# Performance work log

Measured on AMD Instinct MI355X. Metric: run time of the kernel, lower is better.

Reference implementation:

```python
import jax, jax.numpy as jnp
import numpy as np

HID, STEM, BN_OUT, STEM_OUT, MLP = 256, 64, 128, 64, 128
BN_WS, STEM_WS = 5, 17
N, H_BN, W_BN, H_VIS, W_VIS = 4096, 128, 128, 1024, 1024


def setup_inputs() -> dict:
    key = jax.random.key(0)
    ks = jax.random.split(key, 24)
    f32 = jnp.float32
    def rn(k, shape, s=0.05):
        return jax.random.normal(k, shape, f32) * s
    return dict(
        bottleneck=rn(ks[0], (1, HID, H_BN, W_BN), 1.0),
        vis_stem_features=rn(ks[1], (1, STEM, H_VIS, W_VIS), 1.0),
        source_positions_vis=jax.random.uniform(ks[2], (N, 2), f32, 10.0, W_VIS - 10.0),
        pixel_to_sky=rn(ks[3], (N, 2, 2), 0.1),
        fused_h=H_BN, fused_w=W_BN, vis_h=H_VIS, vis_w=W_VIS,
        dw_w=rn(ks[4], (HID, 1, 7, 7)), dw_b=rn(ks[5], (HID,)),
        ln_g=jnp.ones((HID,), f32), ln_b=jnp.zeros((HID,), f32),
        pw1_w=rn(ks[6], (4 * HID, HID)), pw1_b=rn(ks[7], (4 * HID,)),
        pw2_w=rn(ks[8], (HID, 4 * HID)), pw2_b=rn(ks[9], (HID,)),
        cn_gamma=jnp.full((HID,), 1e-2, f32),
        bn1x1_w=rn(ks[10], (BN_OUT, HID, 1, 1)), bn1x1_b=rn(ks[11], (BN_OUT,)),
        st1_w=rn(ks[12], (STEM_OUT, STEM, 3, 3)), st1_b=rn(ks[13], (STEM_OUT,)),
        st2_w=rn(ks[14], (STEM_OUT, STEM_OUT, 3, 3)), st2_b=rn(ks[15], (STEM_OUT,)),
        h1_w=rn(ks[16], (MLP, BN_OUT + STEM_OUT)), h1_b=rn(ks[17], (MLP,)),
        h2_w=rn(ks[18], (MLP, MLP)), h2_b=rn(ks[19], (MLP,)),
        h3_w=rn(ks[20], (3, MLP)),
        h3_b=jnp.array([0.0, 0.0, float(np.log(0.05))], f32),
    )


def _gelu(x):
    return jax.nn.gelu(x, approximate=False)


def _conv2d(x, w, b, padding, groups=1):
    y = jax.lax.conv_general_dilated(
        x, w, (1, 1), [(padding, padding), (padding, padding)],
        dimension_numbers=('NCHW', 'OIHW', 'NCHW'), feature_group_count=groups)
    return y + b[None, :, None, None]


def _bilinear_windows(fm, pos, ws):
    """fm [1,C,H,W], pos [N,2] pixel coords -> [N,C,ws,ws].
    Matches torch grid_sample(mode=bilinear, padding=zeros, align_corners=True)
    with the module's normalize/unnormalize, i.e. direct pixel-coord sampling."""
    C, H, W = fm.shape[1:]
    fm2 = fm[0]
    half = ws // 2
    off = jnp.arange(-half, half + 1, dtype=pos.dtype)
    gy, gx = jnp.meshgrid(off, off, indexing='ij')
    xs = gx[None] + pos[:, 0, None, None]   # [N,ws,ws]
    ys = gy[None] + pos[:, 1, None, None]
    x0 = jnp.floor(xs); y0 = jnp.floor(ys)
    wx1 = xs - x0; wy1 = ys - y0
    x0i = x0.astype(jnp.int32); y0i = y0.astype(jnp.int32)
    def gather(yi, xi, w):
        valid = (yi >= 0) & (yi < H) & (xi >= 0) & (xi < W)
        v = fm2[:, jnp.clip(yi, 0, H - 1), jnp.clip(xi, 0, W - 1)]  # [C,N,ws,ws]
        return v * (w * valid)[None]
    out = (gather(y0i, x0i, (1 - wy1) * (1 - wx1))
           + gather(y0i, x0i + 1, (1 - wy1) * wx1)
           + gather(y0i + 1, x0i, wy1 * (1 - wx1))
           + gather(y0i + 1, x0i + 1, wy1 * wx1))
    return jnp.transpose(out, (1, 0, 2, 3))


def _gauss(ws):
    t = jnp.linspace(-1.0, 1.0, ws)
    yy, xx = jnp.meshgrid(t, t, indexing='ij')
    g = jnp.exp(-(xx ** 2 + yy ** 2) / (2 * 0.4 ** 2))
    return g / g.sum()


def _convnext(x, dw_w, dw_b, ln_g, ln_b, pw1_w, pw1_b, pw2_w, pw2_b, gamma):
    r = x
    x = _conv2d(x, dw_w, dw_b, padding=3, groups=x.shape[1])  # depthwise 7x7
    mu = x.mean(1, keepdims=True)
    var = ((x - mu) ** 2).mean(1, keepdims=True)
    x = (x - mu) / jnp.sqrt(var + 1e-6)
    x = x * ln_g[None, :, None, None] + ln_b[None, :, None, None]
    x = jnp.einsum('nchw,oc->nohw', x, pw1_w) + pw1_b[None, :, None, None]
    x = _gelu(x)
    x = jnp.einsum('nchw,oc->nohw', x, pw2_w) + pw2_b[None, :, None, None]
    return r + gamma[None, :, None, None] * x


def _forward(bottleneck, vis_stem_features, source_positions_vis, pixel_to_sky,
             dw_w, dw_b, ln_g, ln_b, pw1_w, pw1_b, pw2_w, pw2_b, cn_gamma,
             bn1x1_w, bn1x1_b, st1_w, st1_b, st2_w, st2_b,
             h1_w, h1_b, h2_w, h2_b, h3_w, h3_b,
             fused_h, fused_w, vis_h, vis_w):
    scale = jnp.array([fused_w / vis_w, fused_h / vis_h], source_positions_vis.dtype)
    pos_bn = source_positions_vis * scale
    # bottleneck branch: 5x5 windows -> ConvNeXt -> 1x1 conv -> GELU -> gauss pool
    bn_win = _bilinear_windows(bottleneck, pos_bn, BN_WS)              # [N,256,5,5]
    bn_feat = _convnext(bn_win, dw_w, dw_b, ln_g, ln_b, pw1_w, pw1_b, pw2_w, pw2_b, cn_gamma)
    bn_feat = _gelu(_conv2d(bn_feat, bn1x1_w, bn1x1_b, padding=0))     # [N,128,5,5]
    bn_vec = (bn_feat * _gauss(BN_WS)[None, None]).sum((-2, -1))       # [N,128]
    st_win = _bilinear_windows(vis_stem_features, source_positions_vis, STEM_WS)
    st = _gelu(_conv2d(st_win, st1_w, st1_b, padding=1))
    st = _gelu(_conv2d(st, st2_w, st2_b, padding=1))                   # [N,64,17,17]
    st_vec = (st * _gauss(STEM_WS)[None, None]).sum((-2, -1))          # [N,64]
    # head MLP
    x = jnp.concatenate([bn_vec, st_vec], axis=1)                      # [N,192]
    x = _gelu(x @ h1_w.T + h1_b)
    x = _gelu(x @ h2_w.T + h2_b)
    out = x @ h3_w.T + h3_b                                            # [N,3]
    dx_px, dy_px = out[:, 0], out[:, 1]
    log_sigma = jnp.clip(out[:, 2], -6.0, 3.0)
    pix = jnp.stack([dx_px, dy_px], axis=1)                            # [N,2]
    pred_sky = jnp.einsum('nij,nj->ni', pixel_to_sky, pix)             # [N,2]
    confidence = 1.0 / jnp.maximum(jnp.exp(log_sigma), 1e-4)
    return pred_sky, dx_px, dy_px, log_sigma, confidence


def reference(bottleneck, vis_stem_features, source_positions_vis, pixel_to_sky,
              fused_h, fused_w, vis_h, vis_w,
              dw_w, dw_b, ln_g, ln_b, pw1_w, pw1_b, pw2_w, pw2_b, cn_gamma,
              bn1x1_w, bn1x1_b, st1_w, st1_b, st2_w, st2_b,
              h1_w, h1_b, h2_w, h2_b, h3_w, h3_b):
    return _forward(bottleneck, vis_stem_features, source_positions_vis, pixel_to_sky,
                    dw_w, dw_b, ln_g, ln_b, pw1_w, pw1_b, pw2_w, pw2_b, cn_gamma,
                    bn1x1_w, bn1x1_b, st1_w, st1_b, st2_w, st2_b,
                    h1_w, h1_b, h2_w, h2_b, h3_w, h3_b,
                    fused_h, fused_w, vis_h, vis_w)
```

## Files before the change

### kernel.cpp

```cpp
#include <hip/hip_runtime.h>
#include <hip/hip_bf16.h>

#define XSTR 28

typedef short short8 __attribute__((ext_vector_type(8)));
typedef float f32x4  __attribute__((ext_vector_type(4)));

__device__ __forceinline__ float gelu_f(float x){
    return 0.5f*x*(1.0f + erff(x*0.70710678118654752f));
}
__device__ __forceinline__ float gelu_q(float x){
    const float z = 1.5957691216057308f*x*(1.0f + 0.044715f*x*x);
    return x / (1.0f + __expf(-z));
}
__device__ __forceinline__ unsigned short f2bf(float f){
    unsigned int u = __float_as_uint(f);
    u += 0x7fffu + ((u>>16)&1u);
    return (unsigned short)(u>>16);
}
__device__ __forceinline__ unsigned int pack2(float a, float b){
    return (unsigned int)f2bf(a) | ((unsigned int)f2bf(b)<<16);
}
__device__ __forceinline__ float bf_lo(unsigned int u){ return __uint_as_float(u<<16); }
__device__ __forceinline__ float bf_hi(unsigned int u){ return __uint_as_float(u & 0xffff0000u); }
__device__ __forceinline__ float bfu(unsigned short v){ return __uint_as_float(((unsigned int)v)<<16); }

__device__ __forceinline__ void fma_row25(const float* __restrict__ row, float w, float* __restrict__ acc){
    const float4* r4 = (const float4*)row;
    float4 a0=r4[0], a1=r4[1], a2=r4[2], a3=r4[3], a4=r4[4], a5=r4[5];
    float a6 = row[24];
    acc[0]+=a0.x*w;  acc[1]+=a0.y*w;  acc[2]+=a0.z*w;  acc[3]+=a0.w*w;
    acc[4]+=a1.x*w;  acc[5]+=a1.y*w;  acc[6]+=a1.z*w;  acc[7]+=a1.w*w;
    acc[8]+=a2.x*w;  acc[9]+=a2.y*w;  acc[10]+=a2.z*w; acc[11]+=a2.w*w;
    acc[12]+=a3.x*w; acc[13]+=a3.y*w; acc[14]+=a3.z*w; acc[15]+=a3.w*w;
    acc[16]+=a4.x*w; acc[17]+=a4.y*w; acc[18]+=a4.z*w; acc[19]+=a4.w*w;
    acc[20]+=a5.x*w; acc[21]+=a5.y*w; acc[22]+=a5.z*w; acc[23]+=a5.w*w;
    acc[24]+=a6*w;
}

__global__ __launch_bounds__(512,4) void bn_branch_mfma(
    const float* __restrict__ bottleneck, const float* __restrict__ pos,
    const float* __restrict__ dw_w, const float* __restrict__ dw_b,
    const float* __restrict__ ln_g, const float* __restrict__ ln_b,
    const float* __restrict__ pw1_b, const float* __restrict__ pw2_b,
    const float* __restrict__ cn_gamma, const float* __restrict__ bn1x1_b,
    const short8* __restrict__ P1v, const short8* __restrict__ P2v,
    const short8* __restrict__ Pbv,
    float* __restrict__ vec_out)
{
    __shared__ __align__(16) unsigned char Xb[64*512];
    __shared__ __align__(16) unsigned char Hc[64*256];
    __shared__ float redA[400], redB[400], muS[56], rsS[56];

    const int n0 = blockIdx.x*2, t = threadIdx.x;
    const int lane = t & 63, w = t >> 6;
    const int mcol = lane & 15, h4 = lane >> 4;
    const int sP = t >> 8, cP = t & 255;

    unsigned int wvp[13];
    float xdw[25];
    {
        const int n = n0 + sP;
        const float px = pos[2*n]*0.125f, py = pos[2*n+1]*0.125f;
        const float fpx = floorf(px), fpy = floorf(py);
        const int ix0 = (int)fpx - 2, iy0 = (int)fpy - 2;
        const float fx = px - fpx, fy = py - fpy;
        const float w00=(1.f-fy)*(1.f-fx), w01=(1.f-fy)*fx, w10=fy*(1.f-fx), w11=fy*fx;
        float wv[25];
        {
            const float* fm = bottleneck + cP*16384;
            float P[6][6];
            #pragma unroll
            for (int r=0;r<6;r++){
                const int y = iy0+r;
                const bool yok = (y>=0)&&(y<128);
                const int yc = y<0?0:(y>127?127:y);
                #pragma unroll
                for (int s=0;s<6;s++){
                    const int x = ix0+s;
                    const bool ok = yok && (x>=0) && (x<128);
                    const int xc = x<0?0:(x>127?127:x);
                    P[r][s] = ok ? fm[yc*128+xc] : 0.f;
                }
            }
            #pragma unroll
            for (int a=0;a<5;a++)
            #pragma unroll
            for (int b=0;b<5;b++)
                wv[a*5+b] = w00*P[a][b]+w01*P[a][b+1]+w10*P[a+1][b]+w11*P[a+1][b+1];
        }
        #pragma unroll
        for (int i=0;i<12;i++) wvp[i] = pack2(wv[2*i], wv[2*i+1]);
        wvp[12] = pack2(wv[24], 0.f);
        {
            float wcr[49];
            const float* wc = dw_w + cP*49;
            #pragma unroll
            for (int k=0;k<49;k++) wcr[k]=wc[k];
            const float bb = dw_b[cP];
            #pragma unroll
            for (int i=0;i<5;i++){
                #pragma unroll
                for (int j=0;j<5;j++){
                    float a = bb;
                    #pragma unroll
                    for (int u=0;u<7;u++){
                        const int y = i+u-3;
                        if (y<0||y>4) continue;
                        #pragma unroll
                        for (int v=0;v<7;v++){
                            const int x = j+v-3;
                            if (x<0||x>4) continue;
                            a += wv[y*5+x]*wcr[u*7+v];
                        }
                    }
                    xdw[i*5+j] = a;
                }
            }
        }
        #pragma unroll
        for (int p=0;p<25;p++){
            const int row = sP*32 + p;
            *(unsigned short*)(Xb + row*512 + ((2*cP) ^ ((row&7)<<4))) = f2bf(xdw[p]);
        }
    }
    __syncthreads();
    if (t < 400){
        const int sp = t>>3, part = t&7;
        const int row = (sp/25)*32 + (sp - (sp/25)*25);
        float a=0.f, b=0.f;
        for (int c=part; c<256; c+=8){
            const float v = bfu(*(const unsigned short*)(Xb + row*512 + ((2*c) ^ ((row&7)<<4))));
            a += v; b += v*v;
        }
        redA[t]=a; redB[t]=b;
    }
    __syncthreads();
    if (t < 50){
        float a=0.f, b=0.f;
        #pragma unroll
        for (int s=0;s<8;s++){ a+=redA[t*8+s]; b+=redB[t*8+s]; }
        const float m = a*(1.f/256.f);
        const float var = b*(1.f/256.f) - m*m;
        muS[t]=m; rsS[t]=rsqrtf(var+1e-6f);
    }
    __syncthreads();
    {
        const float g = ln_g[cP], bb = ln_b[cP];
        #pragma unroll
        for (int p=0;p<25;p++){
            const int row = sP*32 + p;
            const float v = (xdw[p]-muS[sP*25+p])*rsS[sP*25+p]*g + bb;
            *(unsigned short*)(Xb + row*512 + ((2*cP) ^ ((row&7)<<4))) = f2bf(v);
        }
    }
    __syncthreads();

    f32x4 acc2[2][4];
    #pragma unroll
    for (int ml=0;ml<2;ml++)
        #pragma unroll
        for (int nt=0;nt<4;nt++) acc2[ml][nt]=0.f;

    for (int ch=0; ch<8; ++ch){
        const int mt = ch*8 + w;
        f32x4 a1[4];
        #pragma unroll
        for (int nt=0;nt<4;nt++) a1[nt]=0.f;
        #pragma unroll
        for (int kk=0; kk<8; ++kk){
            const short8 av = P1v[((mt<<3)+kk)*64 + lane];
            #pragma unroll
            for (int nt=0; nt<4; ++nt){
                const int row = nt*16 + mcol;
                const int ad = row*512 + ((kk*64 + h4*16) ^ ((row&7)<<4));
                const short8 bv = *(const short8*)(Xb + ad);
                a1[nt] = __builtin_amdgcn_mfma_f32_16x16x32_bf16(av, bv, a1[nt], 0,0,0);
            }
        }
        {
            const float4 b1v = *(const float4*)(pw1_b + mt*16 + h4*4);
            #pragma unroll
            for (int nt=0; nt<4; ++nt){
                const int row = nt*16 + mcol;
                const float g0 = gelu_q(a1[nt].x + b1v.x);
                const float g1 = gelu_q(a1[nt].y + b1v.y);
                const float g2 = gelu_q(a1[nt].z + b1v.z);
                const float g3 = gelu_q(a1[nt].w + b1v.w);
                const int ad = row*256 + ((w*32 + h4*8) ^ ((row&7)<<4));
                *(uint2*)(Hc + ad) = make_uint2(pack2(g0,g1), pack2(g2,g3));
            }
        }
        __syncthreads();
        #pragma unroll
        for (int ml=0; ml<2; ++ml){
            const int mtc = w*2 + ml;
            #pragma unroll
            for (int kk2=0; kk2<4; ++kk2){
                const short8 av = P2v[(mtc*32 + (ch*4 + kk2))*64 + lane];
                #pragma unroll
                for (int nt=0; nt<4; ++nt){
                    const int row = nt*16 + mcol;
                    const int ad = row*256 + ((kk2*64 + h4*16) ^ ((row&7)<<4));
                    const short8 bv = *(const short8*)(Hc + ad);
                    acc2[ml][nt] = __builtin_amdgcn_mfma_f32_16x16x32_bf16(av, bv, acc2[ml][nt], 0,0,0);
                }
            }
        }
        __syncthreads();
    }

    #pragma unroll
    for (int ml=0; ml<2; ++ml){
        const int c0 = (w*2+ml)*16 + h4*4;
        const float4 gm = *(const float4*)(cn_gamma + c0);
        const float4 b2 = *(const float4*)(pw2_b + c0);
        #pragma unroll
        for (int nt=0; nt<4; ++nt){
            const int row = nt*16 + mcol;
            const int ad = row*512 + ((2*c0) ^ ((row&7)<<4));
            const float f0 = gm.x*(acc2[ml][nt].x + b2.x);
            const float f1 = gm.y*(acc2[ml][nt].y + b2.y);
            const float f2 = gm.z*(acc2[ml][nt].z + b2.z);
            const float f3 = gm.w*(acc2[ml][nt].w + b2.w);
            *(uint2*)(Xb + ad) = make_uint2(pack2(f0,f1), pack2(f2,f3));
        }
    }
    __syncthreads();
    #pragma unroll
    for (int p=0;p<25;p++){
        const int row = sP*32 + p;
        unsigned short* ptr = (unsigned short*)(Xb + row*512 + ((2*cP) ^ ((row&7)<<4)));
        const float r = (p&1) ? bf_hi(wvp[p>>1]) : bf_lo(wvp[p>>1]);
        *ptr = f2bf(bfu(*ptr) + r);
    }
    __syncthreads();

    {
        f32x4 a3[4];
        #pragma unroll
        for (int nt=0;nt<4;nt++) a3[nt]=0.f;
        #pragma unroll
        for (int kk=0; kk<8; ++kk){
            const short8 av = Pbv[((w<<3)+kk)*64 + lane];
            #pragma unroll
            for (int nt=0; nt<4; ++nt){
                const int row = nt*16 + mcol;
                const int ad = row*512 + ((kk*64 + h4*16) ^ ((row&7)<<4));
                const short8 bv = *(const short8*)(Xb + ad);
                a3[nt] = __builtin_amdgcn_mfma_f32_16x16x32_bf16(av, bv, a3[nt], 0,0,0);
            }
        }
        const float4 bb = *(const float4*)(bn1x1_b + w*16 + h4*4);
        float e5[5];
        #pragma unroll
        for (int a=0;a<5;a++){
            const float ta = -1.f + 0.5f*a;
            e5[a] = expf(-3.125f*ta*ta);
        }
        const float Sv = e5[0]+e5[1]+e5[2]+e5[3]+e5[4];
        const float invS = 1.0f/(Sv*Sv);
        float sA[2][4];
        #pragma unroll
        for (int s=0;s<2;s++)
            #pragma unroll
            for (int j=0;j<4;j++) sA[s][j]=0.f;
        #pragma unroll
        for (int nt=0; nt<4; ++nt){
            const int row = nt*16 + mcol;
            const int s = row>>5, p = row&31;
            if (p < 25){
                const int pa = p/5, pb = p - pa*5;
                const float g = e5[pa]*e5[pb];
                sA[s][0] += g*gelu_q(a3[nt].x + bb.x);
                sA[s][1] += g*gelu_q(a3[nt].y + bb.y);
                sA[s][2] += g*gelu_q(a3[nt].z + bb.z);
                sA[s][3] += g*gelu_q(a3[nt].w + bb.w);
            }
        }
        #pragma unroll
        for (int off=1; off<16; off<<=1){
            #pragma unroll
            for (int s=0;s<2;s++)
                #pragma unroll
                for (int j=0;j<4;j++) sA[s][j] += __shfl_xor(sA[s][j], off);
        }
        if (mcol == 0){
            const int o = w*16 + h4*4;
            #pragma unroll
            for (int s=0;s<2;s++){
                float* vo = vec_out + (n0+s)*192 + o;
                vo[0]=sA[s][0]*invS; vo[1]=sA[s][1]*invS;
                vo[2]=sA[s][2]*invS; vo[3]=sA[s][3]*invS;
            }
        }
    }
}

__global__ __launch_bounds__(256) void prepack_bn_kernel(
    const float* __restrict__ W1, const float* __restrict__ W2, const float* __restrict__ Wb,
    unsigned short* __restrict__ P1, unsigned short* __restrict__ P2, unsigned short* __restrict__ Pb)
{
    const int tid = blockIdx.x*256 + threadIdx.x;
    const float* src; unsigned short* dst; int row, col, stride, idx;
    if (tid < 32768){
        idx = tid;
        const int frag = idx>>6, l = idx&63;
        row = (frag>>3)*16 + (l&15); col = (frag&7)*32 + (l>>4)*8; stride = 256;
        src = W1; dst = P1;
    } else if (tid < 65536){
        idx = tid - 32768;
        const int frag = idx>>6, l = idx&63;
        row = (frag>>5)*16 + (l&15); col = (frag&31)*32 + (l>>4)*8; stride = 1024;
        src = W2; dst = P2;
    } else if (tid < 69632){
        idx = tid - 65536;
        const int frag = idx>>6, l = idx&63;
        row = (frag>>3)*16 + (l&15); col = (frag&7)*32 + (l>>4)*8; stride = 256;
        src = Wb; dst = Pb;
    } else return;
    const float* s = src + row*stride + col;
    unsigned int v[4];
    #pragma unroll
    for (int j=0;j<4;j++) v[j] = pack2(s[2*j], s[2*j+1]);
    *(uint4*)(dst + (size_t)idx*8) = make_uint4(v[0],v[1],v[2],v[3]);
}

__global__ __launch_bounds__(256,2) void bn_branch_valu(
    const float* __restrict__ bottleneck, const float* __restrict__ pos,
    const float* __restrict__ dw_w, const float* __restrict__ dw_b,
    const float* __restrict__ ln_g, const float* __restrict__ ln_b,
    const float* __restrict__ pw1_w, const float* __restrict__ pw1_b,
    const float* __restrict__ pw2_w, const float* __restrict__ pw2_b,
    const float* __restrict__ cn_gamma,
    const float* __restrict__ bn1x1_w, const float* __restrict__ bn1x1_b,
    float* __restrict__ vec_out)
{
    __shared__ float xln[256*XSTR];
    __shared__ float hbuf[256*XSTR];
    __shared__ float redA[200], redB[200];
    __shared__ float mu[25], rs[25];

    const int n = blockIdx.x;
    const int t = threadIdx.x;
    const int c = t;

    const float px = pos[2*n]*0.125f, py = pos[2*n+1]*0.125f;
    const float fpx = floorf(px), fpy = floorf(py);
    const int ix0 = (int)fpx - 2, iy0 = (int)fpy - 2;
    const float fx = px - fpx, fy = py - fpy;
    const float w00=(1.f-fy)*(1.f-fx), w01=(1.f-fy)*fx, w10=fy*(1.f-fx), w11=fy*fx;

    float wv[25];
    {
        const float* fm = bottleneck + c*16384;
        float P[6][6];
        #pragma unroll
        for (int r=0;r<6;r++){
            const int y = iy0+r;
            const bool yok = (y>=0)&&(y<128);
            const int yc = y<0?0:(y>127?127:y);
            #pragma unroll
            for (int s=0;s<6;s++){
                const int x = ix0+s;
                const bool ok = yok && (x>=0) && (x<128);
                const int xc = x<0?0:(x>127?127:x);
                P[r][s] = ok ? fm[yc*128+xc] : 0.f;
            }
        }
        #pragma unroll
        for (int a=0;a<5;a++)
        #pragma unroll
        for (int b=0;b<5;b++)
            wv[a*5+b] = w00*P[a][b]+w01*P[a][b+1]+w10*P[a+1][b]+w11*P[a+1][b+1];
    }
    {
        float wcr[49];
        const float* wc = dw_w + c*49;
        #pragma unroll
        for (int k=0;k<49;k++) wcr[k]=wc[k];
        const float bb = dw_b[c];
        #pragma unroll
        for (int i=0;i<5;i++){
            #pragma unroll
            for (int j=0;j<5;j++){
                float a = bb;
                #pragma unroll
                for (int u=0;u<7;u++){
                    const int y = i+u-3;
                    if (y<0||y>4) continue;
                    #pragma unroll
                    for (int v=0;v<7;v++){
                        const int x = j+v-3;
                        if (x<0||x>4) continue;
                        a += wv[y*5+x]*wcr[u*7+v];
                    }
                }
                xln[c*XSTR + i*5+j] = a;
            }
        }
    }
    __syncthreads();
    if (t < 200){
        const int p = t>>3, s = t&7;
        float a=0.f, b=0.f;
        for (int cc=s; cc<256; cc+=8){
            const float v = xln[cc*XSTR+p];
            a += v; b += v*v;
        }
        redA[t]=a; redB[t]=b;
    }
    __syncthreads();
    if (t < 25){
        float a=0.f, b=0.f;
        #pragma unroll
        for (int s=0;s<8;s++){ a+=redA[t*8+s]; b+=redB[t*8+s]; }
        const float m = a*(1.f/256.f);
        const float var = b*(1.f/256.f) - m*m;
        mu[t]=m; rs[t]=rsqrtf(var+1e-6f);
    }
    __syncthreads();
    {
        const float g = ln_g[c], bb = ln_b[c];
        #pragma unroll
        for (int p=0;p<25;p++)
            xln[c*XSTR+p] = (xln[c*XSTR+p]-mu[p])*rs[p]*g + bb;
    }
    __syncthreads();
    float acc2[25];
    #pragma unroll
    for (int p=0;p<25;p++) acc2[p]=0.f;
    for (int r=0;r<4;r++){
        const int o = r*256 + t;
        float h[25];
        {
            const float b1 = pw1_b[o];
            #pragma unroll
            for (int p=0;p<25;p++) h[p]=b1;
            const float* wr = pw1_w + o*256;
            for (int cc=0;cc<256;cc++)
                fma_row25(xln + cc*XSTR, wr[cc], h);
            #pragma unroll
            for (int p=0;p<25;p++) h[p]=gelu_f(h[p]);
        }
        __syncthreads();
        #pragma unroll
        for (int p=0;p<25;p++) hbuf[t*XSTR+p]=h[p];
        __syncthreads();
        {
            const float* w2 = pw2_w + t*1024 + r*256;
            for (int k=0;k<256;k++)
                fma_row25(hbuf + k*XSTR, w2[k], acc2);
        }
    }
    {
        const float gam = cn_gamma[c], b2 = pw2_b[c];
        #pragma unroll
        for (int p=0;p<25;p++)
            xln[c*XSTR+p] = wv[p] + gam*(acc2[p]+b2);
    }
    __syncthreads();
    if (t < 128){
        float acc[25];
        #pragma unroll
        for (int p=0;p<25;p++) acc[p]=0.f;
        const float* wr = bn1x1_w + t*256;
        for (int cc=0;cc<256;cc++)
            fma_row25(xln + cc*XSTR, wr[cc], acc);
        const float b = bn1x1_b[t];
        float e5[5];
        #pragma unroll
        for (int a=0;a<5;a++){
            const float ta = -1.f + 0.5f*a;
            e5[a] = expf(-3.125f*ta*ta);
        }
        const float Sv = e5[0]+e5[1]+e5[2]+e5[3]+e5[4];
        float res = 0.f;
        #pragma unroll
        for (int a=0;a<5;a++){
            float rowa = 0.f;
            #pragma unroll
            for (int bb=0;bb<5;bb++)
                rowa += e5[bb]*gelu_f(acc[a*5+bb]+b);
            res += e5[a]*rowa;
        }
        vec_out[n*192+t] = res/(Sv*Sv);
    }
}

__global__ __launch_bounds__(256) void prepack_kernel(
    const float* __restrict__ W1, const float* __restrict__ W2,
    unsigned short* __restrict__ Ap)
{
    const int tid = blockIdx.x*256 + threadIdx.x;
    if (tid >= 9216) return;
    int r = tid;
    const int conv = r / 4608; r -= conv*4608;
    const int k = r / 512;     r -= k*512;
    const int s = r / 256;     r -= s*256;
    const int w = r / 64;
    const int l = r - w*64;
    const float* W = conv ? W2 : W1;
    const int o  = w*16 + (l & 15);
    const int c0 = s*32 + (l >> 4)*8;
    unsigned int v[4];
    #pragma unroll
    for (int jj=0; jj<4; jj++){
        const float f0 = W[o*576 + (c0+2*jj  )*9 + k];
        const float f1 = W[o*576 + (c0+2*jj+1)*9 + k];
        v[jj] = pack2(f0, f1);
    }
    uint4* dst = (uint4*)(Ap + (size_t)tid*8);
    *dst = make_uint4(v[0], v[1], v[2], v[3]);
}

#define STEM_CONV_T(SRC, AP)                                                        \
    for (int k=0;k<9;k++){                                                          \
        const short8 a0 = (AP)[k*512       + w*64 + lane];                          \
        const short8 a1 = (AP)[k*512 + 256 + w*64 + lane];                          \
        const unsigned short* trow = sTab + m*171 + k;                              \
        _Pragma("unroll")                                                           \
        for (int nt=0; nt<19; nt++){                                                \
            const int ad0 = ((int)trow[nt*9]) ^ h16;                                \
            const short8 bv0 = *(const short8*)((SRC) + ad0);                       \
            acc[nt] = __builtin_amdgcn_mfma_f32_16x16x32_bf16(a0, bv0, acc[nt], 0,0,0); \
            const short8 bv1 = *(const short8*)((SRC) + (ad0 ^ 64));                \
            acc[nt] = __builtin_amdgcn_mfma_f32_16x16x32_bf16(a1, bv1, acc[nt], 0,0,0); \
        }                                                                           \
    }

__global__ __launch_bounds__(256,2) void stem_branch_kernel(
    const float* __restrict__ vis,
    const float* __restrict__ pos,
    const short8* __restrict__ Ap1,
    const float* __restrict__ st1_b,
    const float* __restrict__ st2_b,
    float* __restrict__ vec_out)
{
    __shared__ __align__(16) unsigned char sXt[290*128];
    __shared__ __align__(16) unsigned char sC1[290*128];
    __shared__ unsigned short sTab[16*171];
    __shared__ float redS[64];

    const int n = blockIdx.x;
    const int t = threadIdx.x;
    const int lane = t & 63;
    const int m = t & 15;
    const int h16 = ((t >> 4) & 3) * 16;
    const int w = t >> 6;

    const float fpx0 = pos[2*n], fpy0 = pos[2*n+1];
    const float fpx = floorf(fpx0), fpy = floorf(fpy0);
    const int ix0 = (int)fpx - 8, iy0 = (int)fpy - 8;
    const float fx = fpx0-fpx, fy = fpy0-fpy;
    const float w00=(1.f-fy)*(1.f-fx), w01=(1.f-fy)*fx, w10=fy*(1.f-fx), w11=fy*fx;

    if (t < 32)      *(unsigned int*)(sXt + 289*128 + t*4) = 0u;
    else if (t < 64) *(unsigned int*)(sC1 + 289*128 + (t-32)*4) = 0u;

    for (int idx = t; idx < 16*171; idx += 256){
        const int mm = idx/171, rem = idx - mm*171;
        const int nt = rem/9, k = rem - nt*9;
        const int p = nt*16 + mm;
        const int py = (p*241)>>12, px = p - py*17;
        const int dyy = k/3 - 1, dxx = k - (k/3)*3 - 1;
        const int y = py+dyy, x = px+dxx;
        const bool ok = ((unsigned)y < 17u) && ((unsigned)x < 17u);
        const int pp = ok ? (y*17+x) : 289;
        sTab[idx] = (unsigned short)(pp*128 + ((pp&7)<<4));
    }

    for (int task = t; task < 64*17; task += 256){
        const int c  = task & 63;
        const int py = task >> 6;
        const float* r0 = vis + c*1048576 + (iy0+py)*1024 + ix0;
        float a[18], b[18];
        #pragma unroll
        for (int kk=0; kk<18; kk++){ a[kk]=r0[kk]; b[kk]=r0[1024+kk]; }
        #pragma unroll
        for (int px=0; px<17; px++){
            const float v = w00*a[px] + w01*a[px+1] + w10*b[px] + w11*b[px+1];
            const int p = py*17 + px;
            *(unsigned short*)(sXt + p*128 + ((2*c) ^ ((p&7)<<4))) = f2bf(v);
        }
    }
    __syncthreads();

    f32x4 acc[19];
    #pragma unroll
    for (int nt=0; nt<19; nt++) acc[nt] = 0.f;
    STEM_CONV_T(sXt, Ap1)

    {
        const int obase = w*16 + (h16>>2);
        const float bo0 = st1_b[obase], bo1 = st1_b[obase+1];
        const float bo2 = st1_b[obase+2], bo3 = st1_b[obase+3];
        #pragma unroll
        for (int nt=0; nt<19; nt++){
            const int p = nt*16 + m;
            if (p < 289){
                const unsigned r01 = pack2(gelu_q(acc[nt].x+bo0), gelu_q(acc[nt].y+bo1));
                const unsigned r23 = pack2(gelu_q(acc[nt].z+bo2), gelu_q(acc[nt].w+bo3));
                const int ad = p*128 + ((2*obase) ^ ((p&7)<<4));
                *(uint2*)(sC1 + ad) = make_uint2(r01, r23);
            }
        }
    }
    __syncthreads();

    const short8* Ap2 = Ap1 + 4608;
    #pragma unroll
    for (int nt=0; nt<19; nt++) acc[nt] = 0.f;
    STEM_CONV_T(sC1, Ap2)

    {
        const int obase = w*16 + (h16>>2);
        const float bo0 = st2_b[obase], bo1 = st2_b[obase+1];
        const float bo2 = st2_b[obase+2], bo3 = st2_b[obase+3];
        float s0=0.f, s1=0.f, s2=0.f, s3=0.f;
        #pragma unroll
        for (int nt=0; nt<19; nt++){
            const int p = nt*16 + m;
            if (p < 289){
                const int py = (p*241)>>12;
                const int px = p - py*17;
                const float ty = -1.f + 0.125f*py;
                const float tx = -1.f + 0.125f*px;
                const float g = expf(-3.125f*(ty*ty + tx*tx));
                s0 += g*gelu_q(acc[nt].x+bo0);
                s1 += g*gelu_q(acc[nt].y+bo1);
                s2 += g*gelu_q(acc[nt].z+bo2);
                s3 += g*gelu_q(acc[nt].w+bo3);
            }
        }
        #pragma unroll
        for (int off=1; off<16; off<<=1){
            s0 += __shfl_xor(s0, off);
            s1 += __shfl_xor(s1, off);
            s2 += __shfl_xor(s2, off);
            s3 += __shfl_xor(s3, off);
        }
        if (m == 0){
            redS[obase]   = s0;
            redS[obase+1] = s1;
            redS[obase+2] = s2;
            redS[obase+3] = s3;
        }
    }
    __syncthreads();
    if (t < 64){
        float Sv = 0.f;
        #pragma unroll
        for (int j=0;j<17;j++){
            const float tj = -1.f + 0.125f*j;
            Sv += expf(-3.125f*tj*tj);
        }
        vec_out[n*192+128+t] = redS[t] / (Sv*Sv);
    }
}

__global__ __launch_bounds__(128) void head16_kernel(
    const float* __restrict__ vec, const float* __restrict__ p2s,
    const float* __restrict__ h1_w, const float* __restrict__ h1_b,
    const float* __restrict__ h2_w, const float* __restrict__ h2_b,
    const float* __restrict__ h3_w, const float* __restrict__ h3_b,
    float* __restrict__ out, int N)
{
    __shared__ float v[16][192];
    __shared__ float x1s[16][132];
    __shared__ float x2s[16][132];
    __shared__ float o3s[16][4];
    const int n0 = blockIdx.x*16, t = threadIdx.x;

    for (int idx=t; idx<16*192; idx+=128){
        const int s = idx/192, k = idx - s*192;
        v[s][k] = vec[n0*192 + idx];
    }
    __syncthreads();
    {
        const int o = t;
        float acc[16];
        const float b = h1_b[o];
        #pragma unroll
        for (int s=0;s<16;s++) acc[s]=b;
        const float4* wr = (const float4*)(h1_w + o*192);
        for (int k4=0;k4<48;k4++){
            const float4 wv4 = wr[k4];
            #pragma unroll
            for (int s=0;s<16;s++){
                const float4 vv = *(const float4*)&v[s][k4*4];
                acc[s] += wv4.x*vv.x + wv4.y*vv.y + wv4.z*vv.z + wv4.w*vv.w;
            }
        }
        #pragma unroll
        for (int s=0;s<16;s++) x1s[s][o] = gelu_f(acc[s]);
    }
    __syncthreads();
    {
        const int o = t;
        float acc[16];
        const float b = h2_b[o];
        #pragma unroll
        for (int s=0;s<16;s++) acc[s]=b;
        const float4* wr = (const float4*)(h2_w + o*128);
        for (int k4=0;k4<32;k4++){
            const float4 wv4 = wr[k4];
            #pragma unroll
            for (int s=0;s<16;s++){
                const float4 vv = *(const float4*)&x1s[s][k4*4];
                acc[s] += wv4.x*vv.x + wv4.y*vv.y + wv4.z*vv.z + wv4.w*vv.w;
            }
        }
        #pragma unroll
        for (int s=0;s<16;s++) x2s[s][o] = gelu_f(acc[s]);
    }
    __syncthreads();
    if (t < 48){
        const int j = t>>4, s = t&15;
        float a = h3_b[j];
        const float* wr = h3_w + j*128;
        for (int k=0;k<128;k++) a += x2s[s][k]*wr[k];
        o3s[s][j] = a;
    }
    __syncthreads();
    if (t < 16){
        const int s = t, n = n0 + s;
        const float dx = o3s[s][0], dy = o3s[s][1];
        float ls = o3s[s][2];
        ls = ls < -6.f ? -6.f : (ls > 3.f ? 3.f : ls);
        const float s0 = p2s[n*4+0]*dx + p2s[n*4+1]*dy;
        const float s1 = p2s[n*4+2]*dx + p2s[n*4+3]*dy;
        const float conf = 1.0f/fmaxf(expf(ls), 1e-4f);
        out[2*n]   = s0;
        out[2*n+1] = s1;
        out[2*N+n] = dx;
        out[3*N+n] = dy;
        out[4*N+n] = ls;
        out[5*N+n] = conf;
    }
}

extern "C" void kernel_launch(void* const* d_in, const int* in_sizes, int n_in,
                              void* d_out, int out_size, void* d_ws, size_t ws_size,
                              hipStream_t stream)
{
    (void)n_in; (void)out_size;
    const float* bottleneck = (const float*)d_in[0];
    const float* vis        = (const float*)d_in[1];
    const float* pos        = (const float*)d_in[2];
    const float* p2s        = (const float*)d_in[3];
    const float* dw_w  = (const float*)d_in[8];
    const float* dw_b  = (const float*)d_in[9];
    const float* ln_g  = (const float*)d_in[10];
    const float* ln_b  = (const float*)d_in[11];
    const float* pw1_w = (const float*)d_in[12];
    const float* pw1_b = (const float*)d_in[13];
    const float* pw2_w = (const float*)d_in[14];
    const float* pw2_b = (const float*)d_in[15];
    const float* gam   = (const float*)d_in[16];
    const float* b1w   = (const float*)d_in[17];
    const float* b1b   = (const float*)d_in[18];
    const float* s1w   = (const float*)d_in[19];
    const float* s1b   = (const float*)d_in[20];
    const float* s2w   = (const float*)d_in[21];
    const float* s2b   = (const float*)d_in[22];
    const float* h1w   = (const float*)d_in[23];
    const float* h1b   = (const float*)d_in[24];
    const float* h2w   = (const float*)d_in[25];
    const float* h2b   = (const float*)d_in[26];
    const float* h3w   = (const float*)d_in[27];
    const float* h3b   = (const float*)d_in[28];

    const int N = in_sizes[2]/2;
    float* vec = (float*)d_ws;
    const size_t vec_bytes = (size_t)N*192*sizeof(float);
    unsigned short* Apack = (unsigned short*)((char*)d_ws + vec_bytes);
    unsigned short* P1 = Apack + 73728;
    unsigned short* P2 = P1 + 262144;
    unsigned short* Pb = P2 + 262144;
    const size_t need = vec_bytes + 147456u + (262144u+262144u+32768u)*2u;

    hipMemsetAsync(d_ws, 0, vec_bytes, stream);

    prepack_kernel<<<36, 256, 0, stream>>>(s1w, s2w, Apack);

    if (ws_size >= need){
        prepack_bn_kernel<<<272, 256, 0, stream>>>(pw1_w, pw2_w, b1w, P1, P2, Pb);
        bn_branch_mfma<<<N/2, 512, 0, stream>>>(bottleneck, pos, dw_w, dw_b, ln_g, ln_b,
                                                pw1_b, pw2_b, gam, b1b,
                                                (const short8*)P1, (const short8*)P2, (const short8*)Pb,
                                                vec);
    } else {
        bn_branch_valu<<<N, 256, 0, stream>>>(bottleneck, pos, dw_w, dw_b, ln_g, ln_b,
                                              pw1_w, pw1_b, pw2_w, pw2_b, gam, b1w, b1b, vec);
    }
    stem_branch_kernel<<<N, 256, 0, stream>>>(vis, pos, (const short8*)Apack, s1b, s2b, vec);
    head16_kernel<<<N/16, 128, 0, stream>>>(vec, p2s, h1w, h1b, h2w, h2b, h3w, h3b,
                                            (float*)d_out, N);
}
```

Measured before the change: 866.0 us.

## Switch stem convolutions to 32x32x16 MFMA tiles with output/pixel wave split

```diff
diff --git a/kernel.cpp b/kernel.cpp
--- a/kernel.cpp
+++ b/kernel.cpp
@@ -5,6 +5,7 @@
 
 typedef short short8 __attribute__((ext_vector_type(8)));
 typedef float f32x4  __attribute__((ext_vector_type(4)));
+typedef float f32x16 __attribute__((ext_vector_type(16)));
 
 __device__ __forceinline__ float gelu_f(float x){
     return 0.5f*x*(1.0f + erff(x*0.70710678118654752f));
@@ -494,15 +495,15 @@
 {
     const int tid = blockIdx.x*256 + threadIdx.x;
     if (tid >= 9216) return;
-    int r = tid;
-    const int conv = r / 4608; r -= conv*4608;
-    const int k = r / 512;     r -= k*512;
-    const int s = r / 256;     r -= s*256;
-    const int w = r / 64;
-    const int l = r - w*64;
+    const int conv = tid / 4608;
+    const int r = tid - conv*4608;
+    const int frag = r >> 6, l = r & 63;
+    const int k  = frag >> 3;
+    const int kt = (frag >> 1) & 3;
+    const int wo = frag & 1;
     const float* W = conv ? W2 : W1;
-    const int o  = w*16 + (l & 15);
-    const int c0 = s*32 + (l >> 4)*8;
+    const int o  = wo*32 + (l & 31);
+    const int c0 = kt*16 + (l >> 5)*8;
     unsigned int v[4];
     #pragma unroll
     for (int jj=0; jj<4; jj++){
@@ -510,22 +511,24 @@
         const float f1 = W[o*576 + (c0+2*jj+1)*9 + k];
         v[jj] = pack2(f0, f1);
     }
-    uint4* dst = (uint4*)(Ap + (size_t)tid*8);
-    *dst = make_uint4(v[0], v[1], v[2], v[3]);
-}
-
-#define STEM_CONV_T(SRC, AP)                                                        \
+    *(uint4*)(Ap + (size_t)tid*8) = make_uint4(v[0], v[1], v[2], v[3]);
+}
+
+#define STEM_CONV32(SRC, AP)                                                        \
     for (int k=0;k<9;k++){                                                          \
-        const short8 a0 = (AP)[k*512       + w*64 + lane];                          \
-        const short8 a1 = (AP)[k*512 + 256 + w*64 + lane];                          \
-        const unsigned short* trow = sTab + m*171 + k;                              \
+        const unsigned short* trow = sTab + m*90 + nh*45 + k;                       \
+        int tj[5];                                                                  \
         _Pragma("unroll")                                                           \
-        for (int nt=0; nt<19; nt++){                                                \
-            const int ad0 = ((int)trow[nt*9]) ^ h16;                                \
-            const short8 bv0 = *(const short8*)((SRC) + ad0);                       \
-            acc[nt] = __builtin_amdgcn_mfma_f32_16x16x32_bf16(a0, bv0, acc[nt], 0,0,0); \
-            const short8 bv1 = *(const short8*)((SRC) + (ad0 ^ 64));                \
-            acc[nt] = __builtin_amdgcn_mfma_f32_16x16x32_bf16(a1, bv1, acc[nt], 0,0,0); \
+        for (int j=0;j<5;j++) tj[j] = trow[j*9];                                    \
+        _Pragma("unroll")                                                           \
+        for (int kt=0;kt<4;kt++){                                                   \
+            const short8 av = (AP)[(k*8 + kt*2 + wo)*64 + lane];                    \
+            const int cb = kt*32 + hi16;                                            \
+            _Pragma("unroll")                                                       \
+            for (int j=0;j<5;j++){                                                  \
+                const short8 bv = *(const short8*)((SRC) + (tj[j] ^ cb));           \
+                acc[j] = __builtin_amdgcn_mfma_f32_32x32x16_bf16(av, bv, acc[j], 0,0,0); \
+            }                                                                       \
         }                                                                           \
     }
 
@@ -539,15 +542,18 @@
 {
     __shared__ __align__(16) unsigned char sXt[290*128];
     __shared__ __align__(16) unsigned char sC1[290*128];
-    __shared__ unsigned short sTab[16*171];
-    __shared__ float redS[64];
+    __shared__ unsigned short sTab[32*90];
+    __shared__ float redS[64][2];
 
     const int n = blockIdx.x;
     const int t = threadIdx.x;
     const int lane = t & 63;
-    const int m = t & 15;
-    const int h16 = ((t >> 4) & 3) * 16;
+    const int m = lane & 31;
+    const int hi = lane >> 5;
+    const int hi16 = hi*16;
     const int w = t >> 6;
+    const int wo = w & 1;
+    const int nh = w >> 1;
 
     const float fpx0 = pos[2*n], fpy0 = pos[2*n+1];
     const float fpx = floorf(fpx0), fpy = floorf(fpy0);
@@ -558,15 +564,16 @@
     if (t < 32)      *(unsigned int*)(sXt + 289*128 + t*4) = 0u;
     else if (t < 64) *(unsigned int*)(sC1 + 289*128 + (t-32)*4) = 0u;
 
-    for (int idx = t; idx < 16*171; idx += 256){
-        const int mm = idx/171, rem = idx - mm*171;
+    for (int idx = t; idx < 32*90; idx += 256){
+        const int mm = idx/90, rem = idx - mm*90;
         const int nt = rem/9, k = rem - nt*9;
-        const int p = nt*16 + mm;
-        const int py = (p*241)>>12, px = p - py*17;
-        const int dyy = k/3 - 1, dxx = k - (k/3)*3 - 1;
-        const int y = py+dyy, x = px+dxx;
-        const bool ok = ((unsigned)y < 17u) && ((unsigned)x < 17u);
-        const int pp = ok ? (y*17+x) : 289;
+        const int p = nt*32 + mm;
+        int pp = 289;
+        if (p < 289){
+            const int py = (p*241)>>12, px = p - py*17;
+            const int y = py + k/3 - 1, x = px + (k - (k/3)*3) - 1;
+            if (((unsigned)y < 17u) && ((unsigned)x < 17u)) pp = y*17 + x;
+        }
         sTab[idx] = (unsigned short)(pp*128 + ((pp&7)<<4));
     }
 
@@ -586,23 +593,29 @@
     }
     __syncthreads();
 
-    f32x4 acc[19];
+    f32x16 acc[5];
     #pragma unroll
-    for (int nt=0; nt<19; nt++) acc[nt] = 0.f;
-    STEM_CONV_T(sXt, Ap1)
-
-    {
-        const int obase = w*16 + (h16>>2);
-        const float bo0 = st1_b[obase], bo1 = st1_b[obase+1];
-        const float bo2 = st1_b[obase+2], bo3 = st1_b[obase+3];
-        #pragma unroll
-        for (int nt=0; nt<19; nt++){
-            const int p = nt*16 + m;
+    for (int j=0;j<5;j++) acc[j] = 0.f;
+    STEM_CONV32(sXt, Ap1)
+
+    {
+        float4 b4[4];
+        #pragma unroll
+        for (int rg=0;rg<4;rg++) b4[rg] = *(const float4*)(st1_b + wo*32 + 8*rg + 4*hi);
+        #pragma unroll
+        for (int j=0;j<5;j++){
+            const int p = (nh*5+j)*32 + m;
             if (p < 289){
-                const unsigned r01 = pack2(gelu_q(acc[nt].x+bo0), gelu_q(acc[nt].y+bo1));
-                const unsigned r23 = pack2(gelu_q(acc[nt].z+bo2), gelu_q(acc[nt].w+bo3));
-                const int ad = p*128 + ((2*obase) ^ ((p&7)<<4));
-                *(uint2*)(sC1 + ad) = make_uint2(r01, r23);
+                const int swz = (p&7)<<4;
+                #pragma unroll
+                for (int rg=0;rg<4;rg++){
+                    const int ch0 = wo*32 + 8*rg + 4*hi;
+                    const float v0 = gelu_q(acc[j][4*rg+0] + b4[rg].x);
+                    const float v1 = gelu_q(acc[j][4*rg+1] + b4[rg].y);
+                    const float v2 = gelu_q(acc[j][4*rg+2] + b4[rg].z);
+                    const float v3 = gelu_q(acc[j][4*rg+3] + b4[rg].w);
+                    *(uint2*)(sC1 + p*128 + ((2*ch0) ^ swz)) = make_uint2(pack2(v0,v1), pack2(v2,v3));
+                }
             }
         }
     }
@@ -610,41 +623,45 @@
 
     const short8* Ap2 = Ap1 + 4608;
     #pragma unroll
-    for (int nt=0; nt<19; nt++) acc[nt] = 0.f;
-    STEM_CONV_T(sC1, Ap2)
-
-    {
-        const int obase = w*16 + (h16>>2);
-        const float bo0 = st2_b[obase], bo1 = st2_b[obase+1];
-        const float bo2 = st2_b[obase+2], bo3 = st2_b[obase+3];
-        float s0=0.f, s1=0.f, s2=0.f, s3=0.f;
-        #pragma unroll
-        for (int nt=0; nt<19; nt++){
-            const int p = nt*16 + m;
+    for (int j=0;j<5;j++) acc[j] = 0.f;
+    STEM_CONV32(sC1, Ap2)
+
+    {
+        float4 b4[4];
+        #pragma unroll
+        for (int rg=0;rg<4;rg++) b4[rg] = *(const float4*)(st2_b + wo*32 + 8*rg + 4*hi);
+        float s[16];
+        #pragma unroll
+        for (int r=0;r<16;r++) s[r]=0.f;
+        #pragma unroll
+        for (int j=0;j<5;j++){
+            const int p = (nh*5+j)*32 + m;
             if (p < 289){
                 const int py = (p*241)>>12;
                 const int px = p - py*17;
                 const float ty = -1.f + 0.125f*py;
                 const float tx = -1.f + 0.125f*px;
                 const float g = expf(-3.125f*(ty*ty + tx*tx));
-                s0 += g*gelu_q(acc[nt].x+bo0);
-                s1 += g*gelu_q(acc[nt].y+bo1);
-                s2 += g*gelu_q(acc[nt].z+bo2);
-                s3 += g*gelu_q(acc[nt].w+bo3);
-            }
-        }
-        #pragma unroll
-        for (int off=1; off<16; off<<=1){
-            s0 += __shfl_xor(s0, off);
-            s1 += __shfl_xor(s1, off);
-            s2 += __shfl_xor(s2, off);
-            s3 += __shfl_xor(s3, off);
+                #pragma unroll
+                for (int rg=0;rg<4;rg++){
+                    s[4*rg+0] += g*gelu_q(acc[j][4*rg+0] + b4[rg].x);
+                    s[4*rg+1] += g*gelu_q(acc[j][4*rg+1] + b4[rg].y);
+                    s[4*rg+2] += g*gelu_q(acc[j][4*rg+2] + b4[rg].z);
+                    s[4*rg+3] += g*gelu_q(acc[j][4*rg+3] + b4[rg].w);
+                }
+            }
+        }
+        #pragma unroll
+        for (int off=1; off<32; off<<=1){
+            #pragma unroll
+            for (int r=0;r<16;r++) s[r] += __shfl_xor(s[r], off);
         }
         if (m == 0){
-            redS[obase]   = s0;
-            redS[obase+1] = s1;
-            redS[obase+2] = s2;
-            redS[obase+3] = s3;
+            #pragma unroll
+            for (int rg=0;rg<4;rg++)
+                #pragma unroll
+                for (int e=0;e<4;e++)
+                    redS[wo*32 + 8*rg + 4*hi + e][nh] = s[4*rg+e];
         }
     }
     __syncthreads();
@@ -655,7 +672,7 @@
             const float tj = -1.f + 0.125f*j;
             Sv += expf(-3.125f*tj*tj);
         }
-        vec_out[n*192+128+t] = redS[t] / (Sv*Sv);
+        vec_out[n*192+128+t] = (redS[t][0] + redS[t][1]) / (Sv*Sv);
     }
 }
 
```

Measured after the change: 824.8 us. -4.8%, faster.
